# Kernel optimization log

Hardware: AMD Instinct MI355X
Metric: run time of the kernel (lower is better)

Reference implementation:

```python
import jax, jax.numpy as jnp
import numpy as np

N = 50000   # nodes
E = 800000  # edges (avg degree 16)
FIN = 128   # input node features
H = 4       # heads (conv1, conv2)
C = 64      # hidden_channels (per-head out dim)
SLOPE = 0.2
LN_EPS = 1e-5


def gatv2(x, src, dst, Wl, bl, Wr, br, att, bo, heads, outc, n):
    # GATv2Conv: e = att . LeakyReLU(x_l[src] + x_r[dst]); segment-softmax over dst; scatter-add alpha * x_l[src]
    xl = (x @ Wl + bl).reshape(n, heads, outc)
    xr = (x @ Wr + br).reshape(n, heads, outc)
    e = jax.nn.leaky_relu(xl[src] + xr[dst], SLOPE)          # [E, H, C]
    score = jnp.einsum('ehc,hc->eh', e, att)                 # [E, H]
    smax = jax.ops.segment_max(score, dst, num_segments=n)   # [N, H]
    ex = jnp.exp(score - smax[dst])
    denom = jax.ops.segment_sum(ex, dst, num_segments=n)
    alpha = ex / (denom[dst] + 1e-16)                        # [E, H]
    out = jax.ops.segment_sum(alpha[:, :, None] * xl[src], dst, num_segments=n)  # [N, H, C]
    return out.reshape(n, heads * outc) + bo                 # concat=True (default)


def layernorm(x, g, b):
    mu = x.mean(-1, keepdims=True)
    var = ((x - mu) ** 2).mean(-1, keepdims=True)
    return (x - mu) * jax.lax.rsqrt(var + LN_EPS) * g + b


def setup_inputs() -> dict:
    key = jax.random.key(0)
    ks = jax.random.split(key, 32)
    f32 = jnp.float32
    def nrm(k, shape, s):
        return jax.random.normal(k, shape, dtype=f32) * s
    inp = {}
    inp['x'] = jax.random.normal(ks[0], (N, FIN), dtype=f32)
    inp['edge_index'] = jax.random.randint(ks[1], (2, E), 0, N, dtype=jnp.int32)
    inp['batch'] = jnp.zeros((N,), dtype=jnp.int32)
    # conv1: 128 -> 4*64
    inp['W1l'] = nrm(ks[2], (FIN, H * C), 1.0 / np.sqrt(FIN))
    inp['b1l'] = jnp.zeros((H * C,), f32)
    inp['W1r'] = nrm(ks[3], (FIN, H * C), 1.0 / np.sqrt(FIN))
    inp['b1r'] = jnp.zeros((H * C,), f32)
    inp['a1'] = nrm(ks[4], (H, C), 1.0 / np.sqrt(C))
    inp['bo1'] = jnp.zeros((H * C,), f32)
    inp['ln1_g'] = jnp.ones((H * C,), f32)
    inp['ln1_b'] = jnp.zeros((H * C,), f32)
    # conv2: 256 -> 4*64
    inp['W2l'] = nrm(ks[5], (H * C, H * C), 1.0 / np.sqrt(H * C))
    inp['b2l'] = jnp.zeros((H * C,), f32)
    inp['W2r'] = nrm(ks[6], (H * C, H * C), 1.0 / np.sqrt(H * C))
    inp['b2r'] = jnp.zeros((H * C,), f32)
    inp['a2'] = nrm(ks[7], (H, C), 1.0 / np.sqrt(C))
    inp['bo2'] = jnp.zeros((H * C,), f32)
    inp['ln2_g'] = jnp.ones((H * C,), f32)
    inp['ln2_b'] = jnp.zeros((H * C,), f32)
    # conv3: 256 -> 1*64 (heads=1)
    inp['W3l'] = nrm(ks[8], (H * C, C), 1.0 / np.sqrt(H * C))
    inp['b3l'] = jnp.zeros((C,), f32)
    inp['W3r'] = nrm(ks[9], (H * C, C), 1.0 / np.sqrt(H * C))
    inp['b3r'] = jnp.zeros((C,), f32)
    inp['a3'] = nrm(ks[10], (1, C), 1.0 / np.sqrt(C))
    inp['bo3'] = jnp.zeros((C,), f32)
    inp['ln3_g'] = jnp.ones((C,), f32)
    inp['ln3_b'] = jnp.zeros((C,), f32)
    # final linear 64 -> 64
    inp['linW'] = nrm(ks[11], (C, C), 1.0 / np.sqrt(C))
    inp['linb'] = jnp.zeros((C,), f32)
    return inp


def reference(x, edge_index, batch,
              W1l, b1l, W1r, b1r, a1, bo1, ln1_g, ln1_b,
              W2l, b2l, W2r, b2r, a2, bo2, ln2_g, ln2_b,
              W3l, b3l, W3r, b3r, a3, bo3, ln3_g, ln3_b,
              linW, linb):
    src, dst = edge_index[0], edge_index[1]
    n = x.shape[0]
    h = gatv2(x, src, dst, W1l, b1l, W1r, b1r, a1, bo1, H, C, n)
    h = layernorm(h, ln1_g, ln1_b)
    h = gatv2(h, src, dst, W2l, b2l, W2r, b2r, a2, bo2, H, C, n)
    h = layernorm(h, ln2_g, ln2_b)
    h = gatv2(h, src, dst, W3l, b3l, W3r, b3r, a3, bo3, 1, C, n)
    h = layernorm(h, ln3_g, ln3_b)
    return h @ linW + linb
```

## Files before the change

kernel.cpp:

```cpp
#include <hip/hip_runtime.h>
#include <math.h>

#define LRELU_SLOPE 0.2f
#define L2E 1.4426950408889634f

typedef __attribute__((ext_vector_type(8))) short bf16x8;
typedef __attribute__((ext_vector_type(4))) float f32x4;
typedef __attribute__((ext_vector_type(2))) float f2;

__device__ __forceinline__ float fast_exp2(float x) {
  float r; asm("v_exp_f32 %0, %1" : "=v"(r) : "v"(x)); return r;
}

template<int CTRL>
__device__ __forceinline__ float dpp_add(float v) {
  int p = __builtin_amdgcn_update_dpp(0, __float_as_int(v), CTRL, 0xF, 0xF, true);
  return v + __int_as_float(p);
}
__device__ __forceinline__ float row16_sum(float v) {
  v = dpp_add<0xB1>(v);
  v = dpp_add<0x4E>(v);
  v = dpp_add<0x124>(v);
  v = dpp_add<0x128>(v);
  return v;
}

__device__ __forceinline__ unsigned short f2bf(float f) {
  unsigned u = __float_as_uint(f);
  return (unsigned short)((u + 0x7FFFu + ((u >> 16) & 1u)) >> 16);
}
__device__ __forceinline__ f2 bfpair(unsigned p) {
  f2 r;
  r.x = __uint_as_float(p << 16);
  r.y = __uint_as_float(p & 0xffff0000u);
  return r;
}

__global__ void wt_cvt_all(
    const float* __restrict__ W1l, const float* __restrict__ W1r,
    const float* __restrict__ W2l, const float* __restrict__ W2r,
    const float* __restrict__ W3l, const float* __restrict__ W3r,
    unsigned short* __restrict__ Wt1l, unsigned short* __restrict__ Wt1r,
    unsigned short* __restrict__ Wt2l, unsigned short* __restrict__ Wt2r,
    unsigned short* __restrict__ Wt3l, unsigned short* __restrict__ Wt3r) {
  const float* W; unsigned short* Wt; int K, N;
  switch (blockIdx.y) {
    case 0: W = W1l; Wt = Wt1l; K = 128; N = 256; break;
    case 1: W = W1r; Wt = Wt1r; K = 128; N = 256; break;
    case 2: W = W2l; Wt = Wt2l; K = 256; N = 256; break;
    case 3: W = W2r; Wt = Wt2r; K = 256; N = 256; break;
    case 4: W = W3l; Wt = Wt3l; K = 256; N = 64;  break;
    default: W = W3r; Wt = Wt3r; K = 256; N = 64; break;
  }
  int i = blockIdx.x * blockDim.x + threadIdx.x;
  int k8s = K / 8;
  int n = i / k8s, k8 = i - n * k8s;
  if (n >= N) return;
  unsigned short tmp[8];
#pragma unroll
  for (int j = 0; j < 8; ++j) tmp[j] = f2bf(W[(size_t)(k8 * 8 + j) * N + n]);
  *(bf16x8*)(Wt + (size_t)n * K + k8 * 8) = *(bf16x8*)tmp;
}

template<int K, bool CVT>
__global__ __launch_bounds__(512) void gemm_dual(
    const void* __restrict__ Xsrc,
    const unsigned short* __restrict__ Wt0, const unsigned short* __restrict__ Wt1,
    const float* __restrict__ bias0, const float* __restrict__ bias1,
    unsigned short* __restrict__ Y0, unsigned short* __restrict__ Y1, int M) {
  constexpr int LDK = K + 8;
  __shared__ unsigned short As[64 * LDK];
  const int t = threadIdx.x, w = t >> 6, l = t & 63;
  const int lr = l & 15, lk = l >> 4;
  const int rowBase = blockIdx.x * 64;

  if constexpr (CVT) {
    const float* Xf = (const float*)Xsrc;
    constexpr int SPR = K / 4;
    constexpr int ITER = (64 * SPR) / 512;
#pragma unroll
    for (int i = 0; i < ITER; ++i) {
      int idx = i * 512 + t;
      int row = idx / SPR, seg = idx - row * SPR;
      int gr = rowBase + row; if (gr >= M) gr = M - 1;
      float4 v = *(const float4*)(Xf + (size_t)gr * K + seg * 4);
      ushort4 o;
      o.x = f2bf(v.x); o.y = f2bf(v.y); o.z = f2bf(v.z); o.w = f2bf(v.w);
      *(ushort4*)(As + row * LDK + seg * 4) = o;
    }
  } else {
    const unsigned short* Xb = (const unsigned short*)Xsrc;
    constexpr int SPR = K / 8;
    constexpr int ITER = (64 * SPR) / 512;
#pragma unroll
    for (int i = 0; i < ITER; ++i) {
      int idx = i * 512 + t;
      int row = idx / SPR, seg = idx - row * SPR;
      int gr = rowBase + row; if (gr >= M) gr = M - 1;
      *(uint4*)(As + row * LDK + seg * 8) = *(const uint4*)(Xb + (size_t)gr * K + seg * 8);
    }
  }
  __syncthreads();

  const int side = w >> 2;
  const int n0 = (w & 3) * 64;
  const unsigned short* Wt = side ? Wt1 : Wt0;
  const float* bias = side ? bias1 : bias0;
  unsigned short* Y = side ? Y1 : Y0;

  f32x4 acc[4][4];
#pragma unroll
  for (int rt = 0; rt < 4; ++rt)
#pragma unroll
    for (int nt = 0; nt < 4; ++nt) acc[rt][nt] = (f32x4){0.f, 0.f, 0.f, 0.f};

  const unsigned short* bp = Wt + (size_t)(n0 + lr) * K + lk * 8;
  const unsigned short* ap = As + lr * LDK + lk * 8;

#pragma unroll
  for (int k0 = 0; k0 < K; k0 += 32) {
    bf16x8 a[4], b[4];
#pragma unroll
    for (int rt = 0; rt < 4; ++rt) a[rt] = *(const bf16x8*)(ap + rt * 16 * LDK + k0);
#pragma unroll
    for (int nt = 0; nt < 4; ++nt) b[nt] = *(const bf16x8*)(bp + nt * 16 * K + k0);
#pragma unroll
    for (int rt = 0; rt < 4; ++rt)
#pragma unroll
      for (int nt = 0; nt < 4; ++nt)
        acc[rt][nt] = __builtin_amdgcn_mfma_f32_16x16x32_bf16(a[rt], b[nt], acc[rt][nt], 0, 0, 0);
  }

#pragma unroll
  for (int nt = 0; nt < 4; ++nt) {
    float bv = bias[n0 + nt * 16 + lr];
#pragma unroll
    for (int rt = 0; rt < 4; ++rt) {
#pragma unroll
      for (int r = 0; r < 4; ++r) {
        int row = rowBase + rt * 16 + lk * 4 + r;
        if (row < M) Y[(size_t)row * 256 + n0 + nt * 16 + lr] = f2bf(acc[rt][nt][r] + bv);
      }
    }
  }
}

template<int K, int RT>
__global__ __launch_bounds__(256) void gemm_mfma2(
    const unsigned short* __restrict__ Xb,
    const unsigned short* __restrict__ Wt0, const unsigned short* __restrict__ Wt1,
    const float* __restrict__ bias0, const float* __restrict__ bias1,
    unsigned short* __restrict__ Y0, unsigned short* __restrict__ Y1, int M, int N) {
  const int nblk = N >> 6;
  const int side = blockIdx.y / nblk;
  const int n0 = (blockIdx.y - side * nblk) * 64;
  const unsigned short* Wt = side ? Wt1 : Wt0;
  const float* bias = side ? bias1 : bias0;
  unsigned short* Y = side ? Y1 : Y0;

  const int t = threadIdx.x, w = t >> 6, l = t & 63;
  const int lr = l & 15, lk = l >> 4;
  const int rowBase = blockIdx.x * (RT * 64) + w * (RT * 16);

  f32x4 acc[RT][4];
#pragma unroll
  for (int rt = 0; rt < RT; ++rt)
#pragma unroll
    for (int nt = 0; nt < 4; ++nt) acc[rt][nt] = (f32x4){0.f, 0.f, 0.f, 0.f};

  const unsigned short* ap[RT];
#pragma unroll
  for (int rt = 0; rt < RT; ++rt) {
    int row = rowBase + rt * 16 + lr;
    if (row >= M) row = M - 1;
    ap[rt] = Xb + (size_t)row * K + lk * 8;
  }
  const unsigned short* bp = Wt + (size_t)(n0 + lr) * K + lk * 8;

#pragma unroll
  for (int k0 = 0; k0 < K; k0 += 32) {
    bf16x8 a[RT], b[4];
#pragma unroll
    for (int rt = 0; rt < RT; ++rt) a[rt] = *(const bf16x8*)(ap[rt] + k0);
#pragma unroll
    for (int nt = 0; nt < 4; ++nt) b[nt] = *(const bf16x8*)(bp + (size_t)nt * 16 * K + k0);
#pragma unroll
    for (int rt = 0; rt < RT; ++rt)
#pragma unroll
      for (int nt = 0; nt < 4; ++nt)
        acc[rt][nt] = __builtin_amdgcn_mfma_f32_16x16x32_bf16(a[rt], b[nt], acc[rt][nt], 0, 0, 0);
  }

#pragma unroll
  for (int nt = 0; nt < 4; ++nt) {
    float bv = bias[n0 + nt * 16 + lr];
#pragma unroll
    for (int rt = 0; rt < RT; ++rt) {
#pragma unroll
      for (int r = 0; r < 4; ++r) {
        int row = rowBase + rt * 16 + lk * 4 + r;
        if (row < M) Y[(size_t)row * N + n0 + nt * 16 + lr] = f2bf(acc[rt][nt][r] + bv);
      }
    }
  }
}

__global__ void hist_deg(const int* __restrict__ dst, int* __restrict__ deg, int Ee) {
  int e = blockIdx.x * blockDim.x + threadIdx.x;
  if (e < Ee) atomicAdd(&deg[dst[e]], 1);
}

__global__ void scan_blk(const int* __restrict__ deg, int* __restrict__ rowptr,
                         int* __restrict__ bsum, int n) {
  __shared__ int sm[256];
  const int b = blockIdx.x, t = threadIdx.x;
  const int i = b * 256 + t;
  const int v = (i < n) ? deg[i] : 0;
  sm[t] = v;
  __syncthreads();
#pragma unroll
  for (int off = 1; off < 256; off <<= 1) {
    int x = (t >= off) ? sm[t - off] : 0;
    __syncthreads();
    sm[t] += x;
    __syncthreads();
  }
  if (i < n) rowptr[i] = sm[t] - v;
  if (t == 255) bsum[b] = sm[255];
}

__global__ void scan_top(const int* __restrict__ bsum, int* __restrict__ boff,
                         int* __restrict__ rowptr, int nb, int n) {
  __shared__ int sm[1024];
  const int t = threadIdx.x;
  const int v = (t < nb) ? bsum[t] : 0;
  sm[t] = v;
  __syncthreads();
#pragma unroll
  for (int off = 1; off < 1024; off <<= 1) {
    int x = (t >= off) ? sm[t - off] : 0;
    __syncthreads();
    sm[t] += x;
    __syncthreads();
  }
  if (t < nb) boff[t] = sm[t] - v;
  if (t == 1023) rowptr[n] = sm[1023];
}

__global__ void scan_add(int* __restrict__ rowptr, const int* __restrict__ boff, int n) {
  int i = blockIdx.x * 256 + threadIdx.x;
  if (i < n) rowptr[i] += boff[blockIdx.x];
}

__global__ void fill_csr(const int* __restrict__ src, const int* __restrict__ dst,
                         const int* __restrict__ rowptr, int* __restrict__ deg,
                         int* __restrict__ csr_src, int Ee) {
  int e = blockIdx.x * blockDim.x + threadIdx.x;
  if (e >= Ee) return;
  int d = dst[e];
  int p = atomicSub(&deg[d], 1) - 1;
  csr_src[rowptr[d] + p] = src[e];
}

__global__ __launch_bounds__(256) void gat_fused4(
    const unsigned short* __restrict__ xlb, const unsigned short* __restrict__ xrb,
    const float* __restrict__ att,
    const int* __restrict__ rowptr, const int* __restrict__ csr_src,
    const float* __restrict__ bo, const float* __restrict__ gam,
    const float* __restrict__ bet, unsigned short* __restrict__ outp, int n) {
  const int t = threadIdx.x;
  const int wv = t >> 6, lane = t & 63;
  const int node = blockIdx.x * 4 + wv;
  if (node >= n) return;
  const int cb = lane * 4;
  const unsigned loff = (unsigned)lane << 3;
  const char* xl8 = (const char*)xlb;

  uint2 xp = *(const uint2*)((const char*)xrb + (((unsigned)node << 9) + loff));
  const f2 xr0 = bfpair(xp.x), xr1 = bfpair(xp.y);
  const float4 a4 = *(const float4*)(att + cb);
  const f2 at0 = {a4.x * L2E, a4.y * L2E};
  const f2 at1 = {a4.z * L2E, a4.w * L2E};

  const int r0 = rowptr[node], r1 = rowptr[node + 1];
  float s = 0.f;
  f2 o0 = {0.f, 0.f}, o1 = {0.f, 0.f};

  if (r0 < r1) {
    const int last = r1 - 1;
#define GOFF(idx) ((((unsigned)csr_src[idx]) << 9) + loff)
    uint2 p0 = *(const uint2*)(xl8 + GOFF(r0));
    uint2 p1 = *(const uint2*)(xl8 + GOFF(min(r0 + 1, last)));
    uint2 p2 = *(const uint2*)(xl8 + GOFF(min(r0 + 2, last)));
    uint2 p3 = *(const uint2*)(xl8 + GOFF(min(r0 + 3, last)));
    for (int i = r0; i < r1; i += 4) {
      const uint2 c0 = p0, c1 = p1, c2 = p2, c3 = p3;
      if (i + 4 < r1) {
        p0 = *(const uint2*)(xl8 + GOFF(min(i + 4, last)));
        p1 = *(const uint2*)(xl8 + GOFF(min(i + 5, last)));
        p2 = *(const uint2*)(xl8 + GOFF(min(i + 6, last)));
        p3 = *(const uint2*)(xl8 + GOFF(min(i + 7, last)));
      }
      const f2 v00 = bfpair(c0.x), v01 = bfpair(c0.y);
      const f2 v10 = bfpair(c1.x), v11 = bfpair(c1.y);
      const f2 v20 = bfpair(c2.x), v21 = bfpair(c2.y);
      const f2 v30 = bfpair(c3.x), v31 = bfpair(c3.y);

      f2 e;
      f2 q0, q1, q2, q3;
      e = v00 + xr0; e = __builtin_elementwise_max(e, e * LRELU_SLOPE); q0 = e * at0;
      e = v01 + xr1; e = __builtin_elementwise_max(e, e * LRELU_SLOPE); q0 += e * at1;
      e = v10 + xr0; e = __builtin_elementwise_max(e, e * LRELU_SLOPE); q1 = e * at0;
      e = v11 + xr1; e = __builtin_elementwise_max(e, e * LRELU_SLOPE); q1 += e * at1;
      e = v20 + xr0; e = __builtin_elementwise_max(e, e * LRELU_SLOPE); q2 = e * at0;
      e = v21 + xr1; e = __builtin_elementwise_max(e, e * LRELU_SLOPE); q2 += e * at1;
      e = v30 + xr0; e = __builtin_elementwise_max(e, e * LRELU_SLOPE); q3 = e * at0;
      e = v31 + xr1; e = __builtin_elementwise_max(e, e * LRELU_SLOPE); q3 += e * at1;

      float s0 = row16_sum(q0.x + q0.y);
      float s1 = row16_sum(q1.x + q1.y);
      float s2 = row16_sum(q2.x + q2.y);
      float s3 = row16_sum(q3.x + q3.y);
      if (i + 1 >= r1) s1 = -INFINITY;
      if (i + 2 >= r1) s2 = -INFINITY;
      if (i + 3 >= r1) s3 = -INFINITY;
      const float w0 = fast_exp2(s0), w1 = fast_exp2(s1);
      const float w2 = fast_exp2(s2), w3 = fast_exp2(s3);
      s += (w0 + w1) + (w2 + w3);
      o0 += v00 * w0; o1 += v01 * w0;
      o0 += v10 * w1; o1 += v11 * w1;
      o0 += v20 * w2; o1 += v21 * w2;
      o0 += v30 * w3; o1 += v31 * w3;
    }
#undef GOFF
  }

  const float inv = 1.f / (s + 1e-16f);
  const float4 b4 = *(const float4*)(bo + cb);
  const float v0 = fmaf(o0.x, inv, b4.x);
  const float v1 = fmaf(o0.y, inv, b4.y);
  const float v2 = fmaf(o1.x, inv, b4.z);
  const float v3 = fmaf(o1.y, inv, b4.w);

  float ls = row16_sum(v0 + v1 + v2 + v3);
  ls += __shfl_xor(ls, 16);
  ls += __shfl_xor(ls, 32);
  const float mu = ls * (1.f / 256.f);
  const float d0 = v0 - mu, d1 = v1 - mu, d2 = v2 - mu, d3 = v3 - mu;
  float q = row16_sum(d0 * d0 + d1 * d1 + d2 * d2 + d3 * d3);
  q += __shfl_xor(q, 16);
  q += __shfl_xor(q, 32);
  const float rs = rsqrtf(q * (1.f / 256.f) + 1e-5f);

  const float4 g4 = *(const float4*)(gam + cb);
  const float4 e4 = *(const float4*)(bet + cb);
  ushort4 res;
  res.x = f2bf(fmaf(d0 * rs, g4.x, e4.x));
  res.y = f2bf(fmaf(d1 * rs, g4.y, e4.y));
  res.z = f2bf(fmaf(d2 * rs, g4.z, e4.z));
  res.w = f2bf(fmaf(d3 * rs, g4.w, e4.w));
  *(ushort4*)((char*)outp + (((unsigned)node << 9) + loff)) = res;
}

__global__ __launch_bounds__(512) void gat1_lin(
    const unsigned short* __restrict__ xlb, const unsigned short* __restrict__ xrb,
    const float* __restrict__ att,
    const int* __restrict__ rowptr, const int* __restrict__ csr_src,
    const float* __restrict__ bo, const float* __restrict__ gam,
    const float* __restrict__ bet,
    const float* __restrict__ linW, const float* __restrict__ linb,
    float* __restrict__ outp, int n) {
  const int t = threadIdx.x;
  const int wv = t >> 6, lane = t & 63;
  const int grp = lane >> 3, c8 = lane & 7;
  __shared__ float lw[64][64];
  __shared__ float hbuf[8][64];
  for (int i = t; i < 4096; i += 512) lw[i >> 6][i & 63] = linW[i];

  const int node = blockIdx.x * 8 + wv;
  const bool active = node < n;
  const int cb = c8 * 8;
  const unsigned loff = (unsigned)c8 << 4;
  const char* xl8 = (const char*)xlb;

  f2 xr2[4];
  int r0 = 0, r1 = 0;
  if (active) {
    uint4 p = *(const uint4*)((const char*)xrb + (((unsigned)node << 7) + loff));
    xr2[0] = bfpair(p.x); xr2[1] = bfpair(p.y); xr2[2] = bfpair(p.z); xr2[3] = bfpair(p.w);
    r0 = rowptr[node];
    r1 = rowptr[node + 1];
  } else {
#pragma unroll
    for (int j = 0; j < 4; ++j) xr2[j] = (f2){0.f, 0.f};
  }
  f2 at2[4];
  {
    float4 a0 = *(const float4*)(att + cb);
    float4 a1 = *(const float4*)(att + cb + 4);
    at2[0] = (f2){a0.x * L2E, a0.y * L2E}; at2[1] = (f2){a0.z * L2E, a0.w * L2E};
    at2[2] = (f2){a1.x * L2E, a1.y * L2E}; at2[3] = (f2){a1.z * L2E, a1.w * L2E};
  }

  float s = 0.f;
  f2 o2[4];
#pragma unroll
  for (int j = 0; j < 4; ++j) o2[j] = (f2){0.f, 0.f};

  uint4 vpk = {0u, 0u, 0u, 0u};
  {
    int i0 = r0 + grp;
    if (i0 < r1) vpk = *(const uint4*)(xl8 + ((((unsigned)csr_src[i0]) << 7) + loff));
  }
  bool valid = (r0 + grp) < r1;

  for (int base = r0; base < r1; base += 8) {
    const uint4 pc = vpk;
    const bool vld = valid;
    int inext = base + 8 + grp;
    valid = inext < r1;
    if (valid) vpk = *(const uint4*)(xl8 + ((((unsigned)csr_src[inext]) << 7) + loff));

    f2 v0 = bfpair(pc.x), v1 = bfpair(pc.y), v2 = bfpair(pc.z), v3 = bfpair(pc.w);
    f2 e0 = v0 + xr2[0]; e0 = __builtin_elementwise_max(e0, e0 * LRELU_SLOPE);
    f2 e1 = v1 + xr2[1]; e1 = __builtin_elementwise_max(e1, e1 * LRELU_SLOPE);
    f2 e2 = v2 + xr2[2]; e2 = __builtin_elementwise_max(e2, e2 * LRELU_SLOPE);
    f2 e3 = v3 + xr2[3]; e3 = __builtin_elementwise_max(e3, e3 * LRELU_SLOPE);
    f2 sc2 = e0 * at2[0];
    sc2 += e1 * at2[1];
    sc2 += e2 * at2[2];
    sc2 += e3 * at2[3];
    float sc = sc2.x + sc2.y;
    sc = dpp_add<0xB1>(sc);
    sc = dpp_add<0x4E>(sc);
    sc += __shfl_xor(sc, 4);
    if (!vld) sc = -INFINITY;
    const float w = fast_exp2(sc);
    s += w;
    o2[0] += v0 * w;
    o2[1] += v1 * w;
    o2[2] += v2 * w;
    o2[3] += v3 * w;
  }

  float o[8] = {o2[0].x, o2[0].y, o2[1].x, o2[1].y, o2[2].x, o2[2].y, o2[3].x, o2[3].y};
#pragma unroll
  for (int off = 8; off < 64; off <<= 1) {
#pragma unroll
    for (int i = 0; i < 8; ++i) o[i] += __shfl_xor(o[i], off);
    s += __shfl_xor(s, off);
  }

  const float inv = 1.f / (s + 1e-16f);
  float val[8];
  {
    float4 b0 = *(const float4*)(bo + cb);
    float4 b1 = *(const float4*)(bo + cb + 4);
    val[0] = fmaf(o[0], inv, b0.x); val[1] = fmaf(o[1], inv, b0.y);
    val[2] = fmaf(o[2], inv, b0.z); val[3] = fmaf(o[3], inv, b0.w);
    val[4] = fmaf(o[4], inv, b1.x); val[5] = fmaf(o[5], inv, b1.y);
    val[6] = fmaf(o[6], inv, b1.z); val[7] = fmaf(o[7], inv, b1.w);
  }

  float ls = 0.f;
#pragma unroll
  for (int i = 0; i < 8; ++i) ls += val[i];
  ls = dpp_add<0xB1>(ls);
  ls = dpp_add<0x4E>(ls);
  ls += __shfl_xor(ls, 4);
  float mu = ls * (1.f / 64.f);
  float d[8], q = 0.f;
#pragma unroll
  for (int i = 0; i < 8; ++i) { d[i] = val[i] - mu; q = fmaf(d[i], d[i], q); }
  q = dpp_add<0xB1>(q);
  q = dpp_add<0x4E>(q);
  q += __shfl_xor(q, 4);
  float var = q * (1.f / 64.f);
  const float rs = rsqrtf(var + 1e-5f);

  if (grp == 0) {
    float4 g0 = *(const float4*)(gam + cb);
    float4 g1 = *(const float4*)(gam + cb + 4);
    float4 e0 = *(const float4*)(bet + cb);
    float4 e1 = *(const float4*)(bet + cb + 4);
    float* hb = &hbuf[wv][cb];
    hb[0] = fmaf(d[0] * rs, g0.x, e0.x); hb[1] = fmaf(d[1] * rs, g0.y, e0.y);
    hb[2] = fmaf(d[2] * rs, g0.z, e0.z); hb[3] = fmaf(d[3] * rs, g0.w, e0.w);
    hb[4] = fmaf(d[4] * rs, g1.x, e1.x); hb[5] = fmaf(d[5] * rs, g1.y, e1.y);
    hb[6] = fmaf(d[6] * rs, g1.z, e1.z); hb[7] = fmaf(d[7] * rs, g1.w, e1.w);
  }
  __syncthreads();

  float acc = linb[lane];
#pragma unroll 8
  for (int k = 0; k < 64; ++k) acc = fmaf(hbuf[wv][k], lw[k][lane], acc);
  if (active) outp[(size_t)node * 64 + lane] = acc;
}

extern "C" void kernel_launch(void* const* d_in, const int* in_sizes, int n_in,
                              void* d_out, int out_size, void* d_ws, size_t ws_size,
                              hipStream_t stream) {
  const float* x    = (const float*)d_in[0];
  const int*   eidx = (const int*)d_in[1];
  const int Nn = in_sizes[0] / 128;
  const int Ee = in_sizes[1] / 2;
  const int* src = eidx;
  const int* dst = eidx + Ee;

  const float* W1l = (const float*)d_in[3];  const float* b1l = (const float*)d_in[4];
  const float* W1r = (const float*)d_in[5];  const float* b1r = (const float*)d_in[6];
  const float* a1  = (const float*)d_in[7];  const float* bo1 = (const float*)d_in[8];
  const float* g1  = (const float*)d_in[9];  const float* be1 = (const float*)d_in[10];
  const float* W2l = (const float*)d_in[11]; const float* b2l = (const float*)d_in[12];
  const float* W2r = (const float*)d_in[13]; const float* b2r = (const float*)d_in[14];
  const float* a2  = (const float*)d_in[15]; const float* bo2 = (const float*)d_in[16];
  const float* g2  = (const float*)d_in[17]; const float* be2 = (const float*)d_in[18];
  const float* W3l = (const float*)d_in[19]; const float* b3l = (const float*)d_in[20];
  const float* W3r = (const float*)d_in[21]; const float* b3r = (const float*)d_in[22];
  const float* a3  = (const float*)d_in[23]; const float* bo3 = (const float*)d_in[24];
  const float* g3  = (const float*)d_in[25]; const float* be3 = (const float*)d_in[26];
  const float* linW = (const float*)d_in[27]; const float* linb = (const float*)d_in[28];

  char* ws = (char*)d_ws;
  unsigned short* xl   = (unsigned short*)ws; ws += (size_t)Nn * 256 * 2;
  unsigned short* xr   = (unsigned short*)ws; ws += (size_t)Nn * 256 * 2;
  unsigned short* Xb   = (unsigned short*)ws; ws += (size_t)Nn * 256 * 2;
  unsigned short* Wt1l = (unsigned short*)ws; ws += 256 * 128 * 2;
  unsigned short* Wt1r = (unsigned short*)ws; ws += 256 * 128 * 2;
  unsigned short* Wt2l = (unsigned short*)ws; ws += 256 * 256 * 2;
  unsigned short* Wt2r = (unsigned short*)ws; ws += 256 * 256 * 2;
  unsigned short* Wt3l = (unsigned short*)ws; ws += 64 * 256 * 2;
  unsigned short* Wt3r = (unsigned short*)ws; ws += 64 * 256 * 2;
  int*   deg    = (int*)ws;    ws += (size_t)Nn * 4;
  int*   rowptr = (int*)ws;    ws += (size_t)(Nn + 1) * 4;
  int*   bsum   = (int*)ws;    ws += 1024 * 4;
  int*   boff   = (int*)ws;    ws += 1024 * 4;
  int*   csr_src= (int*)ws;    ws += (size_t)Ee * 4;

  const int eblk = (Ee + 255) / 256;
  const int nblk = (Nn + 255) / 256;

  hipMemsetAsync(deg, 0, (size_t)Nn * 4, stream);
  hist_deg<<<eblk, 256, 0, stream>>>(dst, deg, Ee);
  wt_cvt_all<<<dim3(32, 6), 256, 0, stream>>>(W1l, W1r, W2l, W2r, W3l, W3r,
                                              Wt1l, Wt1r, Wt2l, Wt2r, Wt3l, Wt3r);
  scan_blk<<<nblk, 256, 0, stream>>>(deg, rowptr, bsum, Nn);
  scan_top<<<1, 1024, 0, stream>>>(bsum, boff, rowptr, nblk, Nn);
  scan_add<<<nblk, 256, 0, stream>>>(rowptr, boff, Nn);
  fill_csr<<<eblk, 256, 0, stream>>>(src, dst, rowptr, deg, csr_src, Ee);

  const int gdblk = (Nn + 63) / 64;

  gemm_dual<128, true><<<gdblk, 512, 0, stream>>>(x, Wt1l, Wt1r, b1l, b1r, xl, xr, Nn);
  gat_fused4<<<(Nn + 3) / 4, 256, 0, stream>>>(xl, xr, a1, rowptr, csr_src, bo1, g1, be1, Xb, Nn);

  gemm_dual<256, false><<<gdblk, 512, 0, stream>>>(Xb, Wt2l, Wt2r, b2l, b2r, xl, xr, Nn);
  gat_fused4<<<(Nn + 3) / 4, 256, 0, stream>>>(xl, xr, a2, rowptr, csr_src, bo2, g2, be2, Xb, Nn);

  gemm_mfma2<256, 1><<<dim3((Nn + 63) / 64, 2), 256, 0, stream>>>(
      Xb, Wt3l, Wt3r, b3l, b3r, xl, xr, Nn, 64);
  gat1_lin<<<(Nn + 7) / 8, 512, 0, stream>>>(xl, xr, a3, rowptr, csr_src, bo3, g3, be3,
                                             linW, linb, (float*)d_out, Nn);
}
```

Measured before the change: 434.8 us.

## Restructure dual GEMM to stage weight strips in LDS and stream activations

The dual projection GEMM used to stage a 64-row activation tile in LDS while every wave read weights from global memory. It now stages a 64-column weight strip in LDS per block and has each wave stream its own 64 activation rows directly from global memory, with the grid spread over 8 column/side strips. The layer-1 fp32-to-bf16 conversion moves into the MFMA loop. The goal is more weight reuse from LDS and no activation staging barrier, but activations are now re-read from global once per column strip (8 times) and the loads are strided per lane.

```diff
diff --git a/kernel.cpp b/kernel.cpp
--- a/kernel.cpp
+++ b/kernel.cpp
@@ -63,72 +63,96 @@
 }
 
 template<int K, bool CVT>
-__global__ __launch_bounds__(512) void gemm_dual(
+__global__ __launch_bounds__(512) void gemm_bstrip(
     const void* __restrict__ Xsrc,
     const unsigned short* __restrict__ Wt0, const unsigned short* __restrict__ Wt1,
     const float* __restrict__ bias0, const float* __restrict__ bias1,
     unsigned short* __restrict__ Y0, unsigned short* __restrict__ Y1, int M) {
   constexpr int LDK = K + 8;
-  __shared__ unsigned short As[64 * LDK];
+  __shared__ unsigned short Bs[64 * LDK];
   const int t = threadIdx.x, w = t >> 6, l = t & 63;
   const int lr = l & 15, lk = l >> 4;
-  const int rowBase = blockIdx.x * 64;
-
-  if constexpr (CVT) {
-    const float* Xf = (const float*)Xsrc;
-    constexpr int SPR = K / 4;
+
+  const int side = blockIdx.y >> 2;
+  const int n0 = (blockIdx.y & 3) * 64;
+  const unsigned short* Wt = side ? Wt1 : Wt0;
+  const float* bias = side ? bias1 : bias0;
+  unsigned short* Y = side ? Y1 : Y0;
+
+  {
+    constexpr int SPR = K / 8;
     constexpr int ITER = (64 * SPR) / 512;
 #pragma unroll
     for (int i = 0; i < ITER; ++i) {
       int idx = i * 512 + t;
       int row = idx / SPR, seg = idx - row * SPR;
-      int gr = rowBase + row; if (gr >= M) gr = M - 1;
-      float4 v = *(const float4*)(Xf + (size_t)gr * K + seg * 4);
-      ushort4 o;
-      o.x = f2bf(v.x); o.y = f2bf(v.y); o.z = f2bf(v.z); o.w = f2bf(v.w);
-      *(ushort4*)(As + row * LDK + seg * 4) = o;
+      *(uint4*)(Bs + row * LDK + seg * 8) =
+          *(const uint4*)(Wt + (size_t)(n0 + row) * K + seg * 8);
+    }
+  }
+  __syncthreads();
+
+  const int rowBase = (blockIdx.x * 8 + w) * 64;
+
+  f32x4 acc[4][4];
+#pragma unroll
+  for (int rt = 0; rt < 4; ++rt)
+#pragma unroll
+    for (int nt = 0; nt < 4; ++nt) acc[rt][nt] = (f32x4){0.f, 0.f, 0.f, 0.f};
+
+  const unsigned short* bs = Bs + lr * LDK + lk * 8;
+
+  if constexpr (CVT) {
+    const float* Xf = (const float*)Xsrc;
+    const float* ap[4];
+#pragma unroll
+    for (int rt = 0; rt < 4; ++rt) {
+      int row = rowBase + rt * 16 + lr;
+      if (row >= M) row = M - 1;
+      ap[rt] = Xf + (size_t)row * K + lk * 8;
+    }
+#pragma unroll
+    for (int k0 = 0; k0 < K; k0 += 32) {
+      bf16x8 a[4], b[4];
+#pragma unroll
+      for (int rt = 0; rt < 4; ++rt) {
+        float4 v0 = *(const float4*)(ap[rt] + k0);
+        float4 v1 = *(const float4*)(ap[rt] + k0 + 4);
+        unsigned short tmp[8];
+        tmp[0] = f2bf(v0.x); tmp[1] = f2bf(v0.y); tmp[2] = f2bf(v0.z); tmp[3] = f2bf(v0.w);
+        tmp[4] = f2bf(v1.x); tmp[5] = f2bf(v1.y); tmp[6] = f2bf(v1.z); tmp[7] = f2bf(v1.w);
+        a[rt] = *(bf16x8*)tmp;
+      }
+#pragma unroll
+      for (int nt = 0; nt < 4; ++nt) b[nt] = *(const bf16x8*)(bs + nt * 16 * LDK + k0);
+#pragma unroll
+      for (int rt = 0; rt < 4; ++rt)
+#pragma unroll
+        for (int nt = 0; nt < 4; ++nt)
+          acc[rt][nt] = __builtin_amdgcn_mfma_f32_16x16x32_bf16(a[rt], b[nt], acc[rt][nt], 0, 0, 0);
     }
   } else {
     const unsigned short* Xb = (const unsigned short*)Xsrc;
-    constexpr int SPR = K / 8;
-    constexpr int ITER = (64 * SPR) / 512;
-#pragma unroll
-    for (int i = 0; i < ITER; ++i) {
-      int idx = i * 512 + t;
-      int row = idx / SPR, seg = idx - row * SPR;
-      int gr = rowBase + row; if (gr >= M) gr = M - 1;
-      *(uint4*)(As + row * LDK + seg * 8) = *(const uint4*)(Xb + (size_t)gr * K + seg * 8);
-    }
-  }
-  __syncthreads();
-
-  const int side = w >> 2;
-  const int n0 = (w & 3) * 64;
-  const unsigned short* Wt = side ? Wt1 : Wt0;
-  const float* bias = side ? bias1 : bias0;
-  unsigned short* Y = side ? Y1 : Y0;
-
-  f32x4 acc[4][4];
-#pragma unroll
-  for (int rt = 0; rt < 4; ++rt)
-#pragma unroll
-    for (int nt = 0; nt < 4; ++nt) acc[rt][nt] = (f32x4){0.f, 0.f, 0.f, 0.f};
-
-  const unsigned short* bp = Wt + (size_t)(n0 + lr) * K + lk * 8;
-  const unsigned short* ap = As + lr * LDK + lk * 8;
-
-#pragma unroll
-  for (int k0 = 0; k0 < K; k0 += 32) {
-    bf16x8 a[4], b[4];
-#pragma unroll
-    for (int rt = 0; rt < 4; ++rt) a[rt] = *(const bf16x8*)(ap + rt * 16 * LDK + k0);
-#pragma unroll
-    for (int nt = 0; nt < 4; ++nt) b[nt] = *(const bf16x8*)(bp + nt * 16 * K + k0);
-#pragma unroll
-    for (int rt = 0; rt < 4; ++rt)
-#pragma unroll
-      for (int nt = 0; nt < 4; ++nt)
-        acc[rt][nt] = __builtin_amdgcn_mfma_f32_16x16x32_bf16(a[rt], b[nt], acc[rt][nt], 0, 0, 0);
+    const unsigned short* ap[4];
+#pragma unroll
+    for (int rt = 0; rt < 4; ++rt) {
+      int row = rowBase + rt * 16 + lr;
+      if (row >= M) row = M - 1;
+      ap[rt] = Xb + (size_t)row * K + lk * 8;
+    }
+#pragma unroll
+    for (int k0 = 0; k0 < K; k0 += 32) {
+      bf16x8 a[4], b[4];
+#pragma unroll
+      for (int rt = 0; rt < 4; ++rt) a[rt] = *(const bf16x8*)(ap[rt] + k0);
+#pragma unroll
+      for (int nt = 0; nt < 4; ++nt) b[nt] = *(const bf16x8*)(bs + nt * 16 * LDK + k0);
+#pragma unroll
+      for (int rt = 0; rt < 4; ++rt)
+#pragma unroll
+        for (int nt = 0; nt < 4; ++nt)
+          acc[rt][nt] = __builtin_amdgcn_mfma_f32_16x16x32_bf16(a[rt], b[nt], acc[rt][nt], 0, 0, 0);
+    }
   }
 
 #pragma unroll
@@ -549,12 +573,12 @@
   scan_add<<<nblk, 256, 0, stream>>>(rowptr, boff, Nn);
   fill_csr<<<eblk, 256, 0, stream>>>(src, dst, rowptr, deg, csr_src, Ee);
 
-  const int gdblk = (Nn + 63) / 64;
-
-  gemm_dual<128, true><<<gdblk, 512, 0, stream>>>(x, Wt1l, Wt1r, b1l, b1r, xl, xr, Nn);
+  const int gbblk = (Nn + 511) / 512;
+
+  gemm_bstrip<128, true><<<dim3(gbblk, 8), 512, 0, stream>>>(x, Wt1l, Wt1r, b1l, b1r, xl, xr, Nn);
   gat_fused4<<<(Nn + 3) / 4, 256, 0, stream>>>(xl, xr, a1, rowptr, csr_src, bo1, g1, be1, Xb, Nn);
 
-  gemm_dual<256, false><<<gdblk, 512, 0, stream>>>(Xb, Wt2l, Wt2r, b2l, b2r, xl, xr, Nn);
+  gemm_bstrip<256, false><<<dim3(gbblk, 8), 512, 0, stream>>>(Xb, Wt2l, Wt2r, b2l, b2r, xl, xr, Nn);
   gat_fused4<<<(Nn + 3) / 4, 256, 0, stream>>>(xl, xr, a2, rowptr, csr_src, bo2, g2, be2, Xb, Nn);
 
   gemm_mfma2<256, 1><<<dim3((Nn + 63) / 64, 2), 256, 0, stream>>>(
```

Result: slower. 444.5 us (+2.2%).
